# Optimization experiments

Hardware: AMD Instinct MI355X
Metric: run time of the kernel (lower is better)

## Reference

```python
import jax, jax.numpy as jnp
import numpy as np

B, L, DIM = 1, 2048, 4096
H, KV, HD = 32, 8, 128
REP = H // KV
SCALE = HD ** -0.5
ROPE_BASE = 10000.0


def rope_traditional(x, offset=0):
    # x: [B, H, L, D] ; traditional RoPE rotates interleaved pairs (x[2i], x[2i+1])
    D = x.shape[-1]
    Lx = x.shape[2]
    pos = jnp.arange(offset, offset + Lx, dtype=jnp.float32)            # [L]
    inv_freq = ROPE_BASE ** (-jnp.arange(0, D, 2, dtype=jnp.float32) / D)  # [D/2]
    ang = pos[:, None] * inv_freq[None, :]                               # [L, D/2]
    c, s = jnp.cos(ang), jnp.sin(ang)
    x1 = x[..., 0::2]
    x2 = x[..., 1::2]
    r1 = x1 * c - x2 * s
    r2 = x1 * s + x2 * c
    return jnp.stack([r1, r2], axis=-1).reshape(x.shape).astype(x.dtype)


def setup_inputs() -> dict:
    key = jax.random.key(0)
    k0, k1, k2, k3, k4 = jax.random.split(key, 5)
    x = jax.random.normal(k0, (B, L, DIM), dtype=jnp.float32)
    wq = jax.random.normal(k1, (DIM, H * HD), dtype=jnp.float32) * 0.02
    wk = jax.random.normal(k2, (DIM, KV * HD), dtype=jnp.float32) * 0.02
    wv = jax.random.normal(k3, (DIM, KV * HD), dtype=jnp.float32) * 0.02
    wo = jax.random.normal(k4, (H * HD, DIM), dtype=jnp.float32) * 0.02
    # additive causal mask (prefill)
    causal = jnp.tril(jnp.ones((L, L), dtype=bool))
    mask = jnp.where(causal, 0.0, -1e9).astype(jnp.float32)
    return {"x": x, "wq": wq, "wk": wk, "wv": wv, "wo": wo, "mask": mask}


def reference(x, wq, wk, wv, wo, mask):
    Bx, Lx, _ = x.shape
    q = (x @ wq).reshape(Bx, Lx, H, HD).transpose(0, 2, 1, 3)   # [B,H,L,hd]
    k = (x @ wk).reshape(Bx, Lx, KV, HD).transpose(0, 2, 1, 3)  # [B,KV,L,hd]
    v = (x @ wv).reshape(Bx, Lx, KV, HD).transpose(0, 2, 1, 3)
    # GQA head repeat (each kv head repeated REP times contiguously)
    k = jnp.repeat(k, REP, axis=1)  # [B,H,L,hd]
    v = jnp.repeat(v, REP, axis=1)
    # RoPE applied after repeat (cache=None branch), offset 0
    q = rope_traditional(q)
    k = rope_traditional(k)
    scores = jnp.einsum("bhld,bhmd->bhlm", q * SCALE, k) + mask  # [B,H,L,L]
    probs = jax.nn.softmax(scores.astype(jnp.float32), axis=-1).astype(scores.dtype)
    out = jnp.einsum("bhlm,bhmd->bhld", probs, v)
    out = out.transpose(0, 2, 1, 3).reshape(Bx, Lx, H * HD)
    return out @ wo, k, v
```

## Files before the change

### kernel.cpp

```cpp
#include <hip/hip_runtime.h>
#include <hip/hip_bf16.h>
#include <math.h>


#define L_SEQ 2048
#define DIM   4096
#define NH    32
#define NKV   8
#define HD    128
#define SCALE 0.08838834764831845f

typedef __bf16 bf16x8 __attribute__((ext_vector_type(8)));
typedef __bf16 bf16x4 __attribute__((ext_vector_type(4)));
typedef __bf16 bf16x2 __attribute__((ext_vector_type(2)));
typedef float  f32x4  __attribute__((ext_vector_type(4)));

__device__ __forceinline__ void gld16(const void* g, void* l) {
  __builtin_amdgcn_global_load_lds(
      (const __attribute__((address_space(1))) void*)g,
      (__attribute__((address_space(3))) void*)l, 16, 0, 0);
}

__global__ void cast_bf16_kernel(const float* __restrict__ in,
                                 __bf16* __restrict__ out, long n4) {
  long i = blockIdx.x * (long)blockDim.x + threadIdx.x;
  if (i >= n4) return;
  float4 f = reinterpret_cast<const float4*>(in)[i];
  bf16x4 o;
  o[0] = (__bf16)f.x; o[1] = (__bf16)f.y; o[2] = (__bf16)f.z; o[3] = (__bf16)f.w;
  reinterpret_cast<bf16x4*>(out)[i] = o;
}

__global__ void tcast_kernel(const float* __restrict__ in0, __bf16* __restrict__ out0,
                             const float* __restrict__ in1, __bf16* __restrict__ out1,
                             int K, int N) {
  __shared__ float tile[32][33];
  const float* in  = blockIdx.z ? in1  : in0;
  __bf16*     out  = blockIdx.z ? out1 : out0;
  int n0 = blockIdx.x * 32, k0 = blockIdx.y * 32;
  int tx = threadIdx.x & 31, ty = threadIdx.x >> 5;
#pragma unroll
  for (int i = 0; i < 4; ++i)
    tile[ty + i * 8][tx] = in[(long)(k0 + ty + i * 8) * N + n0 + tx];
  __syncthreads();
#pragma unroll
  for (int i = 0; i < 4; ++i)
    out[(long)(n0 + ty + i * 8) * K + k0 + tx] = (__bf16)tile[tx][ty + i * 8];
}

template<int TN>
__global__ __launch_bounds__(512, 2) void gemm_t(
    const __bf16* __restrict__ A, const __bf16* __restrict__ B0,
    const __bf16* __restrict__ B1, void* __restrict__ C0, void* __restrict__ C1,
    int M, int N, int K, int mode) {
  constexpr int TNF = TN / 64;
  constexpr int ABY = 128 * 64 * 2;
  constexpr int BBY = TN * 64 * 2;
  constexpr int BUF = ABY + BBY;
  __shared__ char lds[3 * BUF] __attribute__((aligned(16)));
  const __bf16* Bt = blockIdx.z ? B1 : B0;
  void* C = blockIdx.z ? C1 : C0;

  const int nwg = gridDim.x * gridDim.y;
  const int bid = blockIdx.y * gridDim.x + blockIdx.x;
  const int swz = (bid & 7) * (nwg >> 3) + (bid >> 3);
  const int n0 = (swz % gridDim.x) * TN;
  const int m0 = (swz / gridDim.x) * 128;

  const int t = threadIdx.x, wave = t >> 6, lane = t & 63;
  const int quad = lane >> 4, l16 = lane & 15;
  const int wm = (wave >> 2) * 64, wn = (wave & 3) * (TN / 4);

  const int srow = t >> 3;
  const int scol = ((t & 7) ^ (srow & 7)) * 8;
  const __bf16* pa = A  + (long)(m0 + srow) * K + scol;
  const __bf16* pb = Bt + (long)(n0 + srow) * K + scol;
  const long K64 = (long)64 * K;
  const int ldsA = wave * 1024;
  const int ldsB = ABY + wave * 1024;

  int aoff[2][4], boff[2][TN / 64];
#pragma unroll
  for (int ks = 0; ks < 2; ++ks) {
    const int sw = ((ks * 4 + quad) ^ (l16 & 7)) * 16;
#pragma unroll
    for (int i = 0; i < 4; ++i)
      aoff[ks][i] = (wm + i * 16 + l16) * 128 + sw;
#pragma unroll
    for (int i = 0; i < TN / 64; ++i)
      boff[ks][i] = ABY + (wn + i * 16 + l16) * 128 + sw;
  }

  f32x4 acc[4][TN / 64] = {};
  const int nt = K >> 6;

  {
    char* bb = lds;
#pragma unroll
    for (int pt = 0; pt < 2; ++pt) {
#pragma unroll
      for (int r = 0; r < 2; ++r) gld16(pa + r * K64, bb + ldsA + r * 8192);
#pragma unroll
      for (int r = 0; r < TN / 64; ++r) gld16(pb + r * K64, bb + ldsB + r * 8192);
      pa += 64; pb += 64;
      bb += BUF;
    }
  }

  char* cb = lds;
  char* sb = lds + 2 * BUF;

#pragma unroll 1
  for (int kt = 0; kt < nt - 1; ++kt) {
    if constexpr (TN == 256) asm volatile("s_waitcnt vmcnt(6)" ::: "memory");
    else                     asm volatile("s_waitcnt vmcnt(4)" ::: "memory");
    __builtin_amdgcn_s_barrier();
    bf16x8 af[4], bfr[TN / 64];
#pragma unroll
    for (int i = 0; i < 4; ++i) af[i] = *(const bf16x8*)(cb + aoff[0][i]);
#pragma unroll
    for (int i = 0; i < TN / 64; ++i) bfr[i] = *(const bf16x8*)(cb + boff[0][i]);
    if (kt + 2 < nt) {
#pragma unroll
      for (int r = 0; r < 2; ++r) gld16(pa + r * K64, sb + ldsA + r * 8192);
#pragma unroll
      for (int r = 0; r < TN / 64; ++r) gld16(pb + r * K64, sb + ldsB + r * 8192);
      pa += 64; pb += 64;
    }
    __builtin_amdgcn_s_setprio(1);
#pragma unroll
    for (int tm = 0; tm < 4; ++tm)
#pragma unroll
      for (int tn = 0; tn < TN / 64; ++tn)
        acc[tm][tn] = __builtin_amdgcn_mfma_f32_16x16x32_bf16(
            af[tm], bfr[tn], acc[tm][tn], 0, 0, 0);
    __builtin_amdgcn_s_setprio(0);
#pragma unroll
    for (int i = 0; i < 4; ++i) af[i] = *(const bf16x8*)(cb + aoff[1][i]);
#pragma unroll
    for (int i = 0; i < TN / 64; ++i) bfr[i] = *(const bf16x8*)(cb + boff[1][i]);
    __builtin_amdgcn_s_setprio(1);
#pragma unroll
    for (int tm = 0; tm < 4; ++tm)
#pragma unroll
      for (int tn = 0; tn < TN / 64; ++tn)
        acc[tm][tn] = __builtin_amdgcn_mfma_f32_16x16x32_bf16(
            af[tm], bfr[tn], acc[tm][tn], 0, 0, 0);
    __builtin_amdgcn_s_setprio(0);
    cb += BUF; if (cb == lds + 3 * BUF) cb = lds;
    sb += BUF; if (sb == lds + 3 * BUF) sb = lds;
  }

  asm volatile("s_waitcnt vmcnt(0)" ::: "memory");
  __builtin_amdgcn_s_barrier();
  {
    bf16x8 af[4], bfr[TN / 64];
#pragma unroll
    for (int ks = 0; ks < 2; ++ks) {
#pragma unroll
      for (int i = 0; i < 4; ++i) af[i] = *(const bf16x8*)(cb + aoff[ks][i]);
#pragma unroll
      for (int i = 0; i < TN / 64; ++i) bfr[i] = *(const bf16x8*)(cb + boff[ks][i]);
      __builtin_amdgcn_s_setprio(1);
#pragma unroll
      for (int tm = 0; tm < 4; ++tm)
#pragma unroll
        for (int tn = 0; tn < TN / 64; ++tn)
          acc[tm][tn] = __builtin_amdgcn_mfma_f32_16x16x32_bf16(
              af[tm], bfr[tn], acc[tm][tn], 0, 0, 0);
      __builtin_amdgcn_s_setprio(0);
    }
  }

#pragma unroll
  for (int tm = 0; tm < 4; ++tm)
#pragma unroll
    for (int tn = 0; tn < TN / 64; ++tn)
#pragma unroll
      for (int r = 0; r < 4; ++r) {
        int row = m0 + wm + tm * 16 + quad * 4 + r;
        int col = n0 + wn + tn * 16 + l16;
        float v = acc[tm][tn][r];
        if (mode == 0) {
          ((float*)C)[(long)row * N + col] = v;
        } else {
          long idx = ((long)(col >> 7) * L_SEQ + row) * HD + (col & 127);
          ((__bf16*)C)[idx] = (__bf16)v;
        }
      }
}

#define NLOG2_10K 13.287712379549449f

__global__ void rope_q_kernel(__bf16* __restrict__ q ) {
  int idx = blockIdx.x * blockDim.x + threadIdx.x;
  int i = idx & 63, l = (idx >> 6) & 2047, h = idx >> 17;
  if (h >= NH) return;
  long base = ((long)h * L_SEQ + l) * HD + 2 * i;
  bf16x2 x12 = *(bf16x2*)(q + base);
  float x1 = (float)x12[0], x2 = (float)x12[1];
  float inv = exp2f((float)i * (-NLOG2_10K / 64.0f));
  float s, c; __sincosf((float)l * inv, &s, &c);
  bf16x2 o; o[0] = (__bf16)(x1 * c - x2 * s); o[1] = (__bf16)(x1 * s + x2 * c);
  *(bf16x2*)(q + base) = o;
}

__global__ void ropekv_kernel(__bf16* __restrict__ kb ,
                              const __bf16* __restrict__ vb,
                              float* __restrict__ kout ,
                              float* __restrict__ vout) {
  int idx = blockIdx.x * blockDim.x + threadIdx.x;
  int i = idx & 63, l = (idx >> 6) & 2047, kv = idx >> 17;
  if (kv >= NKV) return;
  long base = ((long)kv * L_SEQ + l) * HD + 2 * i;
  bf16x2 x12 = *(bf16x2*)(kb + base);
  float x1 = (float)x12[0], x2 = (float)x12[1];
  float inv = exp2f((float)i * (-NLOG2_10K / 64.0f));
  float s, c; __sincosf((float)l * inv, &s, &c);
  float r1 = x1 * c - x2 * s, r2 = x1 * s + x2 * c;
  bf16x2 o; o[0] = (__bf16)r1; o[1] = (__bf16)r2;
  *(bf16x2*)(kb + base) = o;
  float2 kf; kf.x = r1; kf.y = r2;
  bf16x2 vv = *(const bf16x2*)(vb + base);
  float2 vf; vf.x = (float)vv[0]; vf.y = (float)vv[1];
  long off = (long)(kv * 4) * L_SEQ * HD + (long)l * HD + 2 * i;
#pragma unroll
  for (int rr = 0; rr < 4; ++rr) {
    *(float2*)(kout + off) = kf;
    *(float2*)(vout + off) = vf;
    off += (long)L_SEQ * HD;
  }
}

__global__ void vtrans_kernel(const __bf16* __restrict__ Vh, __bf16* __restrict__ Vt) {
  __shared__ __bf16 tile[64 * 65];
  int kv = blockIdx.z, lb = blockIdx.x * 64, db = blockIdx.y * 64;
  int t = threadIdx.x;
#pragma unroll
  for (int it = 0; it < 2; ++it) {
    int c = it * 256 + t, r = c >> 3, pc = c & 7;
    bf16x8 v = *(const bf16x8*)(Vh + ((long)kv * L_SEQ + lb + r) * HD + db + pc * 8);
#pragma unroll
    for (int e = 0; e < 8; ++e) tile[r * 65 + pc * 8 + e] = v[e];
  }
  __syncthreads();
#pragma unroll
  for (int it = 0; it < 2; ++it) {
    int c = it * 256 + t, r = c >> 3, pc = c & 7;
    bf16x8 v;
#pragma unroll
    for (int e = 0; e < 8; ++e) v[e] = tile[(pc * 8 + e) * 65 + r];
    *(bf16x8*)(Vt + ((long)kv * HD + db + r) * L_SEQ + lb + pc * 8) = v;
  }
}

#define DTHR 8.0f

__global__ __launch_bounds__(256, 2) void attn4_kernel(
    const __bf16* __restrict__ Q, const __bf16* __restrict__ K,
    const __bf16* __restrict__ Vt, __bf16* __restrict__ O ) {
  __shared__ __bf16 Ks[2][64 * 128]  __attribute__((aligned(16)));
  __shared__ __bf16 Vts[2][128 * 64] __attribute__((aligned(16)));
  __shared__ __bf16 Ps[128 * 64]     __attribute__((aligned(16)));

  const int b = blockIdx.x;
  const int kvg = b & 7;
  const int h   = kvg * 4 + ((b >> 3) & 3);
  const int i16 = b >> 5;
  const int qt  = (i16 < 8) ? (15 - i16) : (i16 - 8);
  const int t = threadIdx.x, wave = t >> 6, lane = t & 63;
  const int quad = lane >> 4, l16 = lane & 15;
  const int mw = wave * 32;
  const __bf16* Kh = K  + (long)kvg * L_SEQ * HD;
  const __bf16* Vh = Vt + (long)kvg * HD * L_SEQ;
  const float SL2 = SCALE * 1.44269504f;

  int kr[4], kk[4], vr[4], vk[4];
#pragma unroll
  for (int it = 0; it < 4; ++it) {
    int c = it * 256 + t;
    kr[it] = c >> 4; kk[it] = ((c & 15) ^ (kr[it] & 7)) * 8;
    vr[it] = c >> 3; vk[it] = ((c & 7)  ^ (vr[it] & 7)) * 8;
  }

  const int nchunk = 2 * qt + 2;
  const int jdiag  = 2 * qt;

  int mq[2]; mq[0] = qt * 128 + mw + l16; mq[1] = mq[0] + 16;

  bf16x8 bq[2][4];
#pragma unroll
  for (int g = 0; g < 2; ++g) {
    const __bf16* qrow = Q + ((long)h * L_SEQ + mq[g]) * HD + quad * 8;
#pragma unroll
    for (int d = 0; d < 4; ++d) bq[g][d] = *(const bf16x8*)(qrow + d * 32);
  }

  f32x4 o_acc[2][8] = {};
  float m_run[2] = {-1e30f, -1e30f}, l_run[2] = {0.f, 0.f};

#pragma unroll
  for (int it = 0; it < 4; ++it) {
    gld16(Kh + (long)kr[it] * HD + kk[it],
          (char*)Ks[0] + (size_t)(it * 256 + wave * 64) * 16);
    gld16(Vh + (long)vr[it] * L_SEQ + vk[it],
          (char*)Vts[0] + (size_t)(it * 256 + wave * 64) * 16);
  }

#pragma unroll 1
  for (int j = 0; j < nchunk; ++j) {
    const int cur = j & 1;
    __syncthreads();
    if (j + 1 < nchunk) {
      const int nxt = cur ^ 1;
#pragma unroll
      for (int it = 0; it < 4; ++it) {
        gld16(Kh + (long)((j + 1) * 64 + kr[it]) * HD + kk[it],
              (char*)Ks[nxt] + (size_t)(it * 256 + wave * 64) * 16);
        gld16(Vh + (long)vr[it] * L_SEQ + (j + 1) * 64 + vk[it],
              (char*)Vts[nxt] + (size_t)(it * 256 + wave * 64) * 16);
      }
    }

    f32x4 s[2][4] = {};
#pragma unroll
    for (int dsi = 0; dsi < 4; ++dsi)
#pragma unroll
      for (int tn = 0; tn < 4; ++tn) {
        bf16x8 ak = *(const bf16x8*)((char*)Ks[cur] + (tn * 16 + l16) * 256 +
                                     (((dsi * 4 + quad) ^ (l16 & 7)) * 16));
        s[0][tn] = __builtin_amdgcn_mfma_f32_16x16x32_bf16(ak, bq[0][dsi], s[0][tn], 0, 0, 0);
        s[1][tn] = __builtin_amdgcn_mfma_f32_16x16x32_bf16(ak, bq[1][dsi], s[1][tn], 0, 0, 0);
      }

#pragma unroll
    for (int g = 0; g < 2; ++g) {
#pragma unroll
      for (int tn = 0; tn < 4; ++tn)
#pragma unroll
        for (int r = 0; r < 4; ++r) {
          float v = s[g][tn][r] * SL2;
          if (j >= jdiag && (j * 64 + tn * 16 + quad * 4 + r) > mq[g]) v = -3.0e38f;
          s[g][tn][r] = v;
        }
      float mx = -3.0e38f;
#pragma unroll
      for (int tn = 0; tn < 4; ++tn)
#pragma unroll
        for (int r = 0; r < 4; ++r) mx = fmaxf(mx, s[g][tn][r]);
      mx = fmaxf(mx, __shfl_xor(mx, 16, 64));
      mx = fmaxf(mx, __shfl_xor(mx, 32, 64));

      const bool defer = __all(mx - m_run[g] <= DTHR);
      const float mnew = defer ? m_run[g] : fmaxf(m_run[g], mx);

      float rs = 0.f;
#pragma unroll
      for (int tn = 0; tn < 4; ++tn)
#pragma unroll
        for (int r = 0; r < 4; ++r) {
          float pe = exp2f(s[g][tn][r] - mnew);
          s[g][tn][r] = pe; rs += pe;
        }
      rs += __shfl_xor(rs, 16, 64);
      rs += __shfl_xor(rs, 32, 64);

      if (defer) {
        l_run[g] += rs;
      } else {
        float alpha = exp2f(m_run[g] - mnew);
#pragma unroll
        for (int td = 0; td < 8; ++td)
#pragma unroll
          for (int r = 0; r < 4; ++r) o_acc[g][td][r] *= alpha;
        l_run[g] = l_run[g] * alpha + rs;
        m_run[g] = mnew;
      }

#pragma unroll
      for (int tn = 0; tn < 4; ++tn) {
        bf16x4 pv;
#pragma unroll
        for (int r = 0; r < 4; ++r) pv[r] = (__bf16)s[g][tn][r];
        *(bf16x4*)((char*)Ps + (mw + g * 16 + l16) * 128 +
                   ((tn * 32 + quad * 8) ^ ((l16 & 7) << 4))) = pv;
      }
    }

#pragma unroll
    for (int ks = 0; ks < 2; ++ks) {
      bf16x8 bp0 = *(const bf16x8*)((char*)Ps + (mw + l16) * 128 +
                                    ((ks * 64 + quad * 16) ^ ((l16 & 7) << 4)));
      bf16x8 bp1 = *(const bf16x8*)((char*)Ps + (mw + 16 + l16) * 128 +
                                    ((ks * 64 + quad * 16) ^ ((l16 & 7) << 4)));
#pragma unroll
      for (int td = 0; td < 8; ++td) {
        bf16x8 av = *(const bf16x8*)((char*)Vts[cur] + (td * 16 + l16) * 128 +
                                     (((ks * 4 + quad) ^ (l16 & 7)) * 16));
        o_acc[0][td] = __builtin_amdgcn_mfma_f32_16x16x32_bf16(av, bp0, o_acc[0][td], 0, 0, 0);
        o_acc[1][td] = __builtin_amdgcn_mfma_f32_16x16x32_bf16(av, bp1, o_acc[1][td], 0, 0, 0);
      }
    }
  }

#pragma unroll
  for (int g = 0; g < 2; ++g) {
    float inv_l = 1.0f / l_run[g];
#pragma unroll
    for (int td = 0; td < 8; ++td) {
      bf16x4 ov;
#pragma unroll
      for (int r = 0; r < 4; ++r) ov[r] = (__bf16)(o_acc[g][td][r] * inv_l);
      *(bf16x4*)(O + (long)mq[g] * DIM + h * HD + td * 16 + quad * 4) = ov;
    }
  }
}

extern "C" void kernel_launch(void* const* d_in, const int* in_sizes, int n_in,
                              void* d_out, int out_size, void* d_ws, size_t ws_size,
                              hipStream_t stream) {
  const float* x  = (const float*)d_in[0];
  const float* wq = (const float*)d_in[1];
  const float* wk = (const float*)d_in[2];
  const float* wv = (const float*)d_in[3];
  const float* wo = (const float*)d_in[4];

  float* out   = (float*)d_out;
  float* k_out = out + (long)L_SEQ * DIM;
  float* v_out = k_out + (long)NH * L_SEQ * HD;

  char* ws = (char*)d_ws;
  __bf16* Xb  = (__bf16*)ws; ws += (long)L_SEQ * DIM * 2;
  __bf16* Wqt = (__bf16*)ws; ws += (long)DIM * DIM * 2;
  __bf16* Wkt = (__bf16*)ws; ws += (long)DIM * (NKV * HD) * 2;
  __bf16* Wvt = (__bf16*)ws; ws += (long)DIM * (NKV * HD) * 2;
  __bf16* Wot = (__bf16*)ws; ws += (long)DIM * DIM * 2;
  __bf16* Qh  = (__bf16*)ws; ws += (long)NH * L_SEQ * HD * 2;
  __bf16* Kh  = (__bf16*)ws; ws += (long)NKV * L_SEQ * HD * 2;
  __bf16* Vh  = (__bf16*)ws; ws += (long)NKV * L_SEQ * HD * 2;
  __bf16* Vt  = (__bf16*)ws; ws += (long)NKV * HD * L_SEQ * 2;
  __bf16* Ob  = (__bf16*)ws; ws += (long)L_SEQ * DIM * 2;

  tcast_kernel<<<dim3(DIM / 32, DIM / 32, 1), 256, 0, stream>>>(wq, Wqt, wq, Wqt, DIM, DIM);
  tcast_kernel<<<dim3((NKV * HD) / 32, DIM / 32, 2), 256, 0, stream>>>(wk, Wkt, wv, Wvt, DIM, NKV * HD);
  tcast_kernel<<<dim3(DIM / 32, DIM / 32, 1), 256, 0, stream>>>(wo, Wot, wo, Wot, DIM, DIM);
  {
    long n = (long)L_SEQ * DIM;
    cast_bf16_kernel<<<dim3(n / 1024), 256, 0, stream>>>(x, Xb, n / 4);
  }
  gemm_t<256><<<dim3(DIM / 256, L_SEQ / 128, 1), 512, 0, stream>>>(
      Xb, Wqt, Wqt, Qh, Qh, L_SEQ, DIM, DIM, 2);
  gemm_t<128><<<dim3((NKV * HD) / 128, L_SEQ / 128, 2), 512, 0, stream>>>(
      Xb, Wkt, Wvt, Kh, Vh, L_SEQ, NKV * HD, DIM, 2);
  rope_q_kernel<<<dim3((NH * L_SEQ * 64) / 256), 256, 0, stream>>>(Qh);
  ropekv_kernel<<<dim3((NKV * L_SEQ * 64) / 256), 256, 0, stream>>>(Kh, Vh, k_out, v_out);
  vtrans_kernel<<<dim3(L_SEQ / 64, HD / 64, NKV), 256, 0, stream>>>(Vh, Vt);
  attn4_kernel<<<dim3(512), 256, 0, stream>>>(Qh, Kh, Vt, Ob);
  gemm_t<256><<<dim3(DIM / 256, L_SEQ / 128, 1), 512, 0, stream>>>(
      Ob, Wot, Wot, out, out, L_SEQ, DIM, DIM, 0);
}
```

Measured before the change: 546.1 us.

## Restructure attention pipeline: single-buffered V, split waits, MFMA priority

The attention kernel now double-buffers only K. The V tile for the current chunk is loaded into a single LDS buffer at the start of each iteration, and a partial vmcnt wait plus barrier placed before the PV matmul hides that load behind QK and the softmax. This cuts LDS use, which may help occupancy, and s_setprio raises wave priority around the MFMA sections. The risk is that the V load now sits on the critical path within the iteration, and the barrier count goes up.

```diff
diff --git a/kernel.cpp b/kernel.cpp
--- a/kernel.cpp
+++ b/kernel.cpp
@@ -53,7 +53,6 @@
     const __bf16* __restrict__ A, const __bf16* __restrict__ B0,
     const __bf16* __restrict__ B1, void* __restrict__ C0, void* __restrict__ C1,
     int M, int N, int K, int mode) {
-  constexpr int TNF = TN / 64;
   constexpr int ABY = 128 * 64 * 2;
   constexpr int BBY = TN * 64 * 2;
   constexpr int BUF = ABY + BBY;
@@ -256,11 +255,11 @@
 
 #define DTHR 8.0f
 
-__global__ __launch_bounds__(256, 2) void attn4_kernel(
+__global__ __launch_bounds__(256, 2) void attn5_kernel(
     const __bf16* __restrict__ Q, const __bf16* __restrict__ K,
     const __bf16* __restrict__ Vt, __bf16* __restrict__ O ) {
   __shared__ __bf16 Ks[2][64 * 128]  __attribute__((aligned(16)));
-  __shared__ __bf16 Vts[2][128 * 64] __attribute__((aligned(16)));
+  __shared__ __bf16 Vts[128 * 64]    __attribute__((aligned(16)));
   __shared__ __bf16 Ps[128 * 64]     __attribute__((aligned(16)));
 
   const int b = blockIdx.x;
@@ -300,38 +299,39 @@
   float m_run[2] = {-1e30f, -1e30f}, l_run[2] = {0.f, 0.f};
 
 #pragma unroll
-  for (int it = 0; it < 4; ++it) {
+  for (int it = 0; it < 4; ++it)
     gld16(Kh + (long)kr[it] * HD + kk[it],
           (char*)Ks[0] + (size_t)(it * 256 + wave * 64) * 16);
-    gld16(Vh + (long)vr[it] * L_SEQ + vk[it],
-          (char*)Vts[0] + (size_t)(it * 256 + wave * 64) * 16);
-  }
 
 #pragma unroll 1
   for (int j = 0; j < nchunk; ++j) {
-    const int cur = j & 1;
-    __syncthreads();
+    const int kcur = j & 1;
+    asm volatile("s_waitcnt vmcnt(0)" ::: "memory");
+    __builtin_amdgcn_s_barrier();
+
+#pragma unroll
+    for (int it = 0; it < 4; ++it)
+      gld16(Vh + (long)vr[it] * L_SEQ + j * 64 + vk[it],
+            (char*)Vts + (size_t)(it * 256 + wave * 64) * 16);
     if (j + 1 < nchunk) {
-      const int nxt = cur ^ 1;
-#pragma unroll
-      for (int it = 0; it < 4; ++it) {
+#pragma unroll
+      for (int it = 0; it < 4; ++it)
         gld16(Kh + (long)((j + 1) * 64 + kr[it]) * HD + kk[it],
-              (char*)Ks[nxt] + (size_t)(it * 256 + wave * 64) * 16);
-        gld16(Vh + (long)vr[it] * L_SEQ + (j + 1) * 64 + vk[it],
-              (char*)Vts[nxt] + (size_t)(it * 256 + wave * 64) * 16);
-      }
+              (char*)Ks[kcur ^ 1] + (size_t)(it * 256 + wave * 64) * 16);
     }
 
     f32x4 s[2][4] = {};
+    __builtin_amdgcn_s_setprio(1);
 #pragma unroll
     for (int dsi = 0; dsi < 4; ++dsi)
 #pragma unroll
       for (int tn = 0; tn < 4; ++tn) {
-        bf16x8 ak = *(const bf16x8*)((char*)Ks[cur] + (tn * 16 + l16) * 256 +
+        bf16x8 ak = *(const bf16x8*)((char*)Ks[kcur] + (tn * 16 + l16) * 256 +
                                      (((dsi * 4 + quad) ^ (l16 & 7)) * 16));
         s[0][tn] = __builtin_amdgcn_mfma_f32_16x16x32_bf16(ak, bq[0][dsi], s[0][tn], 0, 0, 0);
         s[1][tn] = __builtin_amdgcn_mfma_f32_16x16x32_bf16(ak, bq[1][dsi], s[1][tn], 0, 0, 0);
       }
+    __builtin_amdgcn_s_setprio(0);
 
 #pragma unroll
     for (int g = 0; g < 2; ++g) {
@@ -387,6 +387,11 @@
       }
     }
 
+    if (j + 1 < nchunk) asm volatile("s_waitcnt vmcnt(4)" ::: "memory");
+    else                asm volatile("s_waitcnt vmcnt(0)" ::: "memory");
+    __builtin_amdgcn_s_barrier();
+
+    __builtin_amdgcn_s_setprio(1);
 #pragma unroll
     for (int ks = 0; ks < 2; ++ks) {
       bf16x8 bp0 = *(const bf16x8*)((char*)Ps + (mw + l16) * 128 +
@@ -395,12 +400,13 @@
                                     ((ks * 64 + quad * 16) ^ ((l16 & 7) << 4)));
 #pragma unroll
       for (int td = 0; td < 8; ++td) {
-        bf16x8 av = *(const bf16x8*)((char*)Vts[cur] + (td * 16 + l16) * 128 +
+        bf16x8 av = *(const bf16x8*)((char*)Vts + (td * 16 + l16) * 128 +
                                      (((ks * 4 + quad) ^ (l16 & 7)) * 16));
         o_acc[0][td] = __builtin_amdgcn_mfma_f32_16x16x32_bf16(av, bp0, o_acc[0][td], 0, 0, 0);
         o_acc[1][td] = __builtin_amdgcn_mfma_f32_16x16x32_bf16(av, bp1, o_acc[1][td], 0, 0, 0);
       }
     }
+    __builtin_amdgcn_s_setprio(0);
   }
 
 #pragma unroll
@@ -455,7 +461,7 @@
   rope_q_kernel<<<dim3((NH * L_SEQ * 64) / 256), 256, 0, stream>>>(Qh);
   ropekv_kernel<<<dim3((NKV * L_SEQ * 64) / 256), 256, 0, stream>>>(Kh, Vh, k_out, v_out);
   vtrans_kernel<<<dim3(L_SEQ / 64, HD / 64, NKV), 256, 0, stream>>>(Vh, Vt);
-  attn4_kernel<<<dim3(512), 256, 0, stream>>>(Qh, Kh, Vt, Ob);
+  attn5_kernel<<<dim3(512), 256, 0, stream>>>(Qh, Kh, Vt, Ob);
   gemm_t<256><<<dim3(DIM / 256, L_SEQ / 128, 1), 512, 0, stream>>>(
       Ob, Wot, Wot, out, out, L_SEQ, DIM, DIM, 0);
 }
```

New measurement: 548.7 us. No clear change (+0.5%).
